# Performance work log

Measured on AMD Instinct MI355X. Metric: run time of the kernel, lower is better.

## Reference

```python
import jax, jax.numpy as jnp
import numpy as np
from functools import partial

D_MODEL = 1024
D_STATE = 16
D_CONV = 4
EXPAND = 2
D_INNER = EXPAND * D_MODEL
B = 2
L = 1024


def setup_inputs() -> dict:
    key = jax.random.key(0)
    ks = jax.random.split(key, 8)
    s = 0.02
    x = jax.random.normal(ks[0], (B, L, D_MODEL), dtype=jnp.float32)
    in_proj_w = jax.random.normal(ks[1], (D_MODEL, 2 * D_INNER), dtype=jnp.float32) * s
    conv_w = jax.random.normal(ks[2], (D_INNER, 1, D_CONV), dtype=jnp.float32) * s  # depthwise [out, in/groups, k]
    conv_b = jnp.zeros((D_INNER,), dtype=jnp.float32)
    x_proj_w = jax.random.normal(ks[3], (D_INNER, 2 * D_STATE), dtype=jnp.float32) * s
    dt_proj_w = jax.random.normal(ks[4], (D_INNER, D_INNER), dtype=jnp.float32) * s
    dt_proj_b = jax.random.normal(ks[5], (D_INNER,), dtype=jnp.float32) * s
    A_log = jnp.log(jnp.tile(jnp.arange(1, D_STATE + 1, dtype=jnp.float32), (D_INNER, 1)))  # [D_INNER, D_STATE]
    D_param = jnp.ones((D_INNER,), dtype=jnp.float32)
    out_proj_w = jax.random.normal(ks[6], (D_INNER, D_MODEL), dtype=jnp.float32) * s
    return {"x": x, "in_proj_w": in_proj_w, "conv_w": conv_w, "conv_b": conv_b,
            "x_proj_w": x_proj_w, "dt_proj_w": dt_proj_w, "dt_proj_b": dt_proj_b,
            "A_log": A_log, "D_param": D_param, "out_proj_w": out_proj_w}


def _selective_scan(u, delta, A, Bx, Cx, D_param):
    # u, delta: [B, L, D_INNER]; A: [D_INNER, N]; Bx, Cx: [B, L, N]
    deltaA = jnp.exp(delta[..., None] * A)                       # [B, L, D, N]
    deltaB_u = delta[..., None] * Bx[:, :, None, :] * u[..., None]  # [B, L, D, N]

    def step(h, inp):
        dA, dBu, c = inp  # dA,dBu: [B, D, N], c: [B, N]
        h = dA * h + dBu
        y = jnp.sum(h * c[:, None, :], axis=-1)  # [B, D]
        return h, y

    h0 = jnp.zeros((u.shape[0], u.shape[2], A.shape[1]), dtype=u.dtype)
    xs = (jnp.swapaxes(deltaA, 0, 1), jnp.swapaxes(deltaB_u, 0, 1), jnp.swapaxes(Cx, 0, 1))
    _, ys = jax.lax.scan(step, h0, xs)  # ys: [L, B, D]
    y = jnp.swapaxes(ys, 0, 1)
    return y + u * D_param


def reference(x, in_proj_w, conv_w, conv_b, x_proj_w, dt_proj_w, dt_proj_b, A_log, D_param, out_proj_w):
    xr = x @ in_proj_w                                   # [B, L, 2*D_INNER]
    u, res = xr[..., :D_INNER], xr[..., D_INNER:]
    # causal depthwise conv1d (padding=D_CONV-1 on the left, truncated to L)
    uc = jnp.swapaxes(u, 1, 2)                            # [B, D_INNER, L]
    uc = jax.lax.conv_general_dilated(
        uc, conv_w, window_strides=(1,), padding=[(D_CONV - 1, 0)],
        dimension_numbers=("NCH", "OIH", "NCH"), feature_group_count=D_INNER)
    uc = uc + conv_b[None, :, None]
    u = jax.nn.silu(jnp.swapaxes(uc, 1, 2))               # [B, L, D_INNER]
    x_dbl = u @ x_proj_w                                  # [B, L, 2*N]
    Bx, Cx = x_dbl[..., :D_STATE], x_dbl[..., D_STATE:]
    delta = jax.nn.softplus(u @ dt_proj_w.T + dt_proj_b)  # [B, L, D_INNER]
    A = -jnp.exp(A_log)
    y = _selective_scan(u, delta, A, Bx, Cx, D_param)
    y = y * jax.nn.silu(res)
    return y @ out_proj_w
```

## Files before the change

### kernel.cpp

```cpp
#include <hip/hip_runtime.h>
#include <math.h>

#define BATCH   2
#define LSEQ    1024
#define DMODEL  1024
#define DSTATE  16
#define DCONV   4
#define DINNER  2048
#define NROWS   (BATCH * LSEQ)

#define LCHUNK  32
#define NCHUNK  32

typedef short  bf16x8 __attribute__((ext_vector_type(8)));
typedef float  f32x4  __attribute__((ext_vector_type(4)));

__device__ __forceinline__ unsigned short f2bf(float f) {
  unsigned int u = __builtin_bit_cast(unsigned int, f);
  u = (u + 0x7fffu + ((u >> 16) & 1u)) >> 16;
  return (unsigned short)u;
}
__device__ __forceinline__ float bf2f(unsigned short h) {
  return __builtin_bit_cast(float, (unsigned int)h << 16);
}
__device__ __forceinline__ float softplus_f(float v) {
  return (v > 20.f) ? v : __logf(1.f + __expf(v));
}

__device__ __forceinline__ void cvt_ew_body(const float* __restrict__ s,
                                            unsigned short* __restrict__ d,
                                            int blk, int tid) {
  int i = blk * 256 + tid;
  float4 v = ((const float4*)s)[i];
  ushort4 o;
  o.x = f2bf(v.x); o.y = f2bf(v.y); o.z = f2bf(v.z); o.w = f2bf(v.w);
  ((ushort4*)d)[i] = o;
}

__device__ __forceinline__ void cvt_tr_body(const float* __restrict__ s,
                                            unsigned short* __restrict__ d,
                                            int R, int C, int c0, int r0,
                                            int tid, float (*T)[33]) {
#pragma unroll
  for (int i = 0; i < 4; ++i) {
    int e = tid + i * 256;
    int r = e >> 5, c = e & 31;
    T[r][c] = s[(size_t)(r0 + r) * C + c0 + c];
  }
  __syncthreads();
#pragma unroll
  for (int i = 0; i < 4; ++i) {
    int e = tid + i * 256;
    int c = e >> 5, r = e & 31;
    d[(size_t)(c0 + c) * R + r0 + r] = f2bf(T[r][c]);
  }
}

__global__ __launch_bounds__(256) void cvt_all(
    const float* __restrict__ x, const float* __restrict__ w_in,
    const float* __restrict__ dt_w, const float* __restrict__ out_w,
    unsigned short* __restrict__ XB, unsigned short* __restrict__ WINB,
    unsigned short* __restrict__ DTWB, unsigned short* __restrict__ OWB) {
  __shared__ float T[32][33];
  const int bid = blockIdx.x;
  const int tid = threadIdx.x;
  if (bid < 2048) {
    cvt_ew_body(x, XB, bid, tid);
  } else if (bid < 6144) {
    int t = bid - 2048;
    cvt_tr_body(w_in, WINB, 1024, 4096, (t & 127) * 32, (t >> 7) * 32, tid, T);
  } else if (bid < 10240) {
    cvt_ew_body(dt_w, DTWB, bid - 6144, tid);
  } else {
    int t = bid - 10240;
    cvt_tr_body(out_w, OWB, 2048, 1024, (t & 31) * 32, (t >> 5) * 32, tid, T);
  }
}

template <int BN>
__global__ __launch_bounds__(512) void mfma_gemm_nt(
    const unsigned short* __restrict__ A, int lda,
    const unsigned short* __restrict__ Bt, int ldb,
    void* __restrict__ C1v, int ld1,
    void* __restrict__ C2v, int ld2, int N1,
    const float* __restrict__ bias,
    int KS, int mode) {
  constexpr int NT = BN / 64;
  __shared__ unsigned short As[8 * 128 * 8];
  __shared__ unsigned short Bs[8 * BN * 8];
  const int tid  = threadIdx.x;
  const int wave = tid >> 6;
  const int lane = tid & 63;
  const int linear = blockIdx.y * gridDim.x + blockIdx.x;
  const int xcd = linear & 7;
  const int pos = linear >> 3;
  const int row0 = (xcd * 2 + (pos & 1)) * 128;
  const int col0 = (pos >> 1) * BN;
  const int wm0 = (wave >> 2) * 64;
  const int wn0 = (wave & 3) * (BN / 4);
  const int kb = blockIdx.z * KS;

  f32x4 acc[4][NT];
#pragma unroll
  for (int i = 0; i < 4; ++i)
#pragma unroll
    for (int j = 0; j < NT; ++j) acc[i][j] = (f32x4){0.f, 0.f, 0.f, 0.f};

  const int lkc = lane >> 4, li = lane & 15;
  const int sw = li & 7;
  for (int k0 = kb; k0 < kb + KS; k0 += 64) {
#pragma unroll
    for (int it = 0; it < 2; ++it) {
      int s = it * 512 + tid;
      int r = s >> 3;
      int kc = (s & 7) ^ (r & 7);
      __builtin_amdgcn_global_load_lds(
          (const __attribute__((address_space(1))) void*)(A + (size_t)(row0 + r) * lda + k0 + kc * 8),
          (__attribute__((address_space(3))) void*)(&As[s * 8]), 16, 0, 0);
    }
#pragma unroll
    for (int it = 0; it < BN / 64; ++it) {
      int s = it * 512 + tid;
      int r = s >> 3;
      int kc = (s & 7) ^ (r & 7);
      __builtin_amdgcn_global_load_lds(
          (const __attribute__((address_space(1))) void*)(Bt + (size_t)(col0 + r) * ldb + k0 + kc * 8),
          (__attribute__((address_space(3))) void*)(&Bs[s * 8]), 16, 0, 0);
    }
    __syncthreads();
#pragma unroll
    for (int half = 0; half < 2; ++half) {
      bf16x8 af[4], bfr[NT];
#pragma unroll
      for (int mt = 0; mt < 4; ++mt) {
        int ra = wm0 + mt * 16 + li;
        af[mt] = *(const bf16x8*)&As[(ra * 8 + ((half * 4 + lkc) ^ sw)) * 8];
      }
#pragma unroll
      for (int nt = 0; nt < NT; ++nt) {
        int rb = wn0 + nt * 16 + li;
        bfr[nt] = *(const bf16x8*)&Bs[(rb * 8 + ((half * 4 + lkc) ^ sw)) * 8];
      }
#pragma unroll
      for (int mt = 0; mt < 4; ++mt)
#pragma unroll
        for (int nt = 0; nt < NT; ++nt)
          acc[mt][nt] = __builtin_amdgcn_mfma_f32_16x16x32_bf16(
              af[mt], bfr[nt], acc[mt][nt], 0, 0, 0);
    }
    __syncthreads();
  }
  const int lq = lane >> 4;
#pragma unroll
  for (int mt = 0; mt < 4; ++mt) {
    int gm0 = row0 + wm0 + mt * 16 + lq * 4;
#pragma unroll
    for (int nt = 0; nt < NT; ++nt) {
      int gn = col0 + wn0 + nt * 16 + li;
      if (mode == 1) {
        if (gn < N1) {
          unsigned short* C1 = (unsigned short*)C1v;
#pragma unroll
          for (int r = 0; r < 4; ++r)
            C1[(size_t)(gm0 + r) * ld1 + gn] = f2bf(acc[mt][nt][r]);
        } else {
          unsigned short* C2 = (unsigned short*)C2v;
#pragma unroll
          for (int r = 0; r < 4; ++r)
            C2[(size_t)(gm0 + r) * ld2 + gn - N1] = f2bf(acc[mt][nt][r]);
        }
      } else {
        float* C1 = (float*)C1v + (size_t)blockIdx.z * (size_t)N1;
#pragma unroll
        for (int r = 0; r < 4; ++r)
          C1[(size_t)(gm0 + r) * ld1 + gn] = acc[mt][nt][r];
      }
    }
  }
}

__global__ __launch_bounds__(256) void out_reduce(
    const float* __restrict__ P, float* __restrict__ out) {
  const size_t SL = (size_t)NROWS * DMODEL;
  size_t i4 = (size_t)blockIdx.x * 256 + threadIdx.x;
  float4 a = ((const float4*)P)[i4];
  float4 b = ((const float4*)(P + SL))[i4];
  ((float4*)out)[i4] = make_float4(a.x + b.x, a.y + b.y, a.z + b.z, a.w + b.w);
}

__global__ __launch_bounds__(256) void conv_xproj(
    const unsigned short* __restrict__ UPREB, const float* __restrict__ cw,
    const float* __restrict__ cb, const float* __restrict__ W,
    unsigned short* __restrict__ UB, float* __restrict__ XPART) {
  const int ks = blockIdx.x;
  const int rt = blockIdx.y;
  const int row0 = rt * 16;
  const int kbase = ks * 256;
  __shared__ unsigned short sU[16][256];
  __shared__ float Bv[256 * 32];
  const int tid = threadIdx.x;

  for (int i = tid; i < 256 * 32; i += 256)
    Bv[i] = W[(size_t)(kbase + (i >> 5)) * 32 + (i & 31)];

  {
    const int d = kbase + tid;
    const float w0 = cw[d * DCONV + 0], w1 = cw[d * DCONV + 1];
    const float w2 = cw[d * DCONV + 2], w3 = cw[d * DCONV + 3];
    const float bias = cb[d];
    float x0, x1, x2;
    if ((row0 & (LSEQ - 1)) == 0) {
      x0 = x1 = x2 = 0.f;
    } else {
      x0 = bf2f(UPREB[(size_t)(row0 - 3) * DINNER + d]);
      x1 = bf2f(UPREB[(size_t)(row0 - 2) * DINNER + d]);
      x2 = bf2f(UPREB[(size_t)(row0 - 1) * DINNER + d]);
    }
    for (int r = 0; r < 16; ++r) {
      float x3 = bf2f(UPREB[(size_t)(row0 + r) * DINNER + d]);
      float a = bias + x0 * w0 + x1 * w1 + x2 * w2 + x3 * w3;
      float u = a / (1.f + __expf(-a));
      unsigned short ub = f2bf(u);
      sU[r][tid] = ub;
      UB[(size_t)(row0 + r) * DINNER + d] = ub;
      x0 = x1; x1 = x2; x2 = x3;
    }
  }
  __syncthreads();

  const int col = tid & 31, rg = tid >> 5;
  float acc[2] = {};
  for (int k = 0; k < 256; k += 2) {
    float b0 = Bv[k * 32 + col], b1 = Bv[(k + 1) * 32 + col];
#pragma unroll
    for (int rr = 0; rr < 2; ++rr) {
      ushort2 uv = *(const ushort2*)&sU[rg * 2 + rr][k];
      acc[rr] += bf2f(uv.x) * b0 + bf2f(uv.y) * b1;
    }
  }
#pragma unroll
  for (int rr = 0; rr < 2; ++rr)
    XPART[(size_t)ks * NROWS * 32 + (size_t)(row0 + rg * 2 + rr) * 32 + col] = acc[rr];
}

__global__ __launch_bounds__(256) void scan_pass1(
    const float* __restrict__ DT4, const float* __restrict__ dtb,
    const unsigned short* __restrict__ UB,
    const float* __restrict__ XPART, float* __restrict__ BCb,
    const float* __restrict__ A_log,
    float* __restrict__ PBUF, float* __restrict__ HBUF,
    unsigned short* __restrict__ DELTAB) {
  const int bx = blockIdx.x;
  const int b = bx >> 8;
  const int c = (bx >> 3) & (NCHUNK - 1);
  const int d = ((bx & 7) << 8) + threadIdx.x;
  const int l0 = c * LCHUNK;
  const size_t SL = (size_t)NROWS * DINNER;
  __shared__ float sB[LCHUNK * DSTATE];
#pragma unroll
  for (int i = 0; i < 2; ++i) {
    int e = threadIdx.x + i * 256;
    int row = e >> 4, col = e & 15;
    size_t base = (size_t)(b * LSEQ + l0 + row) * 32 + col;
    float s = 0.f;
#pragma unroll
    for (int ks = 0; ks < 8; ++ks) s += XPART[(size_t)ks * NROWS * 32 + base];
    sB[e] = s;
  }
  if ((bx & 7) == 0) {
#pragma unroll
    for (int i = 0; i < 4; ++i) {
      int e = threadIdx.x + i * 256;
      int row = e >> 5, col = e & 31;
      size_t base = (size_t)(b * LSEQ + l0 + row) * 32 + col;
      float s = 0.f;
#pragma unroll
      for (int ks = 0; ks < 8; ++ks) s += XPART[(size_t)ks * NROWS * 32 + base];
      BCb[base] = s;
    }
  }
  const float dtb_v = dtb[d];
  float Avv[DSTATE];
#pragma unroll
  for (int n = 0; n < DSTATE; ++n) Avv[n] = -__expf(A_log[d * DSTATE + n]);
  float h[DSTATE], P[DSTATE];
#pragma unroll
  for (int n = 0; n < DSTATE; ++n) { h[n] = 0.f; P[n] = 1.f; }
  __syncthreads();
  for (int lc = 0; lc < LCHUNK; ++lc) {
    size_t off = ((size_t)(b * LSEQ + l0 + lc)) * DINNER + d;
    float pre = DT4[off] + DT4[off + SL] + DT4[off + 2 * SL] + DT4[off + 3 * SL];
    unsigned short db = f2bf(softplus_f(pre + dtb_v));
    DELTAB[off] = db;
    float delta = bf2f(db);
    float du = delta * bf2f(UB[off]);
#pragma unroll
    for (int n = 0; n < DSTATE; ++n) {
      float dA = __expf(delta * Avv[n]);
      P[n] *= dA;
      h[n] = dA * h[n] + du * sB[lc * DSTATE + n];
    }
  }
  size_t base = ((size_t)(b * NCHUNK + c)) * DSTATE * DINNER + d;
#pragma unroll
  for (int n = 0; n < DSTATE; ++n) {
    PBUF[base + (size_t)n * DINNER] = P[n];
    HBUF[base + (size_t)n * DINNER] = h[n];
  }
}

__global__ __launch_bounds__(256) void scan_combine(
    const float* __restrict__ PBUF, float* __restrict__ HBUF) {
  const int bx = blockIdx.x;
  const int b = bx >> 7;
  const int n = (bx >> 3) & (DSTATE - 1);
  const int d = ((bx & 7) << 8) + threadIdx.x;
  float h = 0.f;
  for (int c = 0; c < NCHUNK; ++c) {
    size_t idx = (((size_t)(b * NCHUNK + c)) * DSTATE + n) * DINNER + d;
    float p = PBUF[idx];
    float hl = HBUF[idx];
    HBUF[idx] = h;
    h = p * h + hl;
  }
}

__global__ __launch_bounds__(256) void scan_pass2(
    const unsigned short* __restrict__ DELTAB, const unsigned short* __restrict__ UB,
    const float* __restrict__ BC, const float* __restrict__ HBUF,
    const float* __restrict__ A_log, const float* __restrict__ D_param,
    const unsigned short* __restrict__ RESB, unsigned short* __restrict__ YB) {
  const int bx = blockIdx.x;
  const int b = bx >> 8;
  const int c = (bx >> 3) & (NCHUNK - 1);
  const int d = ((bx & 7) << 8) + threadIdx.x;
  const int l0 = c * LCHUNK;
  __shared__ float sBC[LCHUNK * 32];
#pragma unroll
  for (int i = 0; i < 4; ++i) {
    int e = threadIdx.x + i * 256;
    sBC[e] = BC[((size_t)(b * LSEQ + l0 + (e >> 5))) * 32 + (e & 31)];
  }
  float Avv[DSTATE];
#pragma unroll
  for (int n = 0; n < DSTATE; ++n) Avv[n] = -__expf(A_log[d * DSTATE + n]);
  const float Dp = D_param[d];
  float h[DSTATE];
  size_t base = ((size_t)(b * NCHUNK + c)) * DSTATE * DINNER + d;
#pragma unroll
  for (int n = 0; n < DSTATE; ++n) h[n] = HBUF[base + (size_t)n * DINNER];
  __syncthreads();
  for (int lc = 0; lc < LCHUNK; ++lc) {
    size_t off = ((size_t)(b * LSEQ + l0 + lc)) * DINNER + d;
    float delta = bf2f(DELTAB[off]);
    float uu = bf2f(UB[off]);
    float du = delta * uu;
    float y = 0.f;
#pragma unroll
    for (int n = 0; n < DSTATE; ++n) {
      float dA = __expf(delta * Avv[n]);
      h[n] = dA * h[n] + du * sBC[lc * 32 + n];
      y += h[n] * sBC[lc * 32 + 16 + n];
    }
    y += uu * Dp;
    float r = bf2f(RESB[off]);
    YB[off] = f2bf(y * (r / (1.f + __expf(-r))));
  }
}

extern "C" void kernel_launch(void* const* d_in, const int* in_sizes, int n_in,
                              void* d_out, int out_size, void* d_ws, size_t ws_size,
                              hipStream_t stream) {
  const float* x       = (const float*)d_in[0];
  const float* w_in    = (const float*)d_in[1];
  const float* conv_w  = (const float*)d_in[2];
  const float* conv_b  = (const float*)d_in[3];
  const float* xproj_w = (const float*)d_in[4];
  const float* dt_w    = (const float*)d_in[5];
  const float* dt_b    = (const float*)d_in[6];
  const float* A_log   = (const float*)d_in[7];
  const float* D_par   = (const float*)d_in[8];
  const float* out_w   = (const float*)d_in[9];
  float* out = (float*)d_out;

  char* ws = (char*)d_ws;
  const size_t MB = 1024 * 1024;
  unsigned short* UPREB  = (unsigned short*)(ws + 0 * MB);
  unsigned short* RESB   = (unsigned short*)(ws + 8 * MB);
  unsigned short* UB     = (unsigned short*)(ws + 16 * MB);
  unsigned short* DELTAB = (unsigned short*)(ws + 24 * MB);
  unsigned short* YB     = (unsigned short*)(ws + 32 * MB);
  unsigned short* XB     = (unsigned short*)(ws + 40 * MB);
  unsigned short* WINB   = (unsigned short*)(ws + 44 * MB);
  unsigned short* DTWB   = (unsigned short*)(ws + 52 * MB);
  unsigned short* OWB    = (unsigned short*)(ws + 60 * MB);
  float* PBUF  = (float*)(ws + 0 * MB);
  float* HBUF  = (float*)(ws + 40 * MB);
  float* BCb   = (float*)(ws + 48 * MB);
  float* XPART = (float*)(ws + 48 * MB + 512 * 1024);
  float* OUT2  = (float*)(ws + 128 * MB);
  float* DT4   = (float*)(ws + 64 * MB);

  cvt_all<<<dim3(12288), dim3(256), 0, stream>>>(
      x, w_in, dt_w, out_w, XB, WINB, DTWB, OWB);
  mfma_gemm_nt<128><<<dim3(2 * DINNER / 128, NROWS / 128, 1), dim3(512), 0, stream>>>(
      XB, DMODEL, WINB, DMODEL, UPREB, DINNER, RESB, DINNER, DINNER,
      nullptr, DMODEL, 1);
  conv_xproj<<<dim3(8, NROWS / 16), dim3(256), 0, stream>>>(
      UPREB, conv_w, conv_b, xproj_w, UB, XPART);
  mfma_gemm_nt<128><<<dim3(DINNER / 128, NROWS / 128, 4), dim3(512), 0, stream>>>(
      UB, DINNER, DTWB, DINNER, DT4, DINNER, nullptr, 0, NROWS * DINNER,
      nullptr, DINNER / 4, 3);
  scan_pass1<<<dim3(BATCH * NCHUNK * (DINNER / 256)), dim3(256), 0, stream>>>(
      DT4, dt_b, UB, XPART, BCb, A_log, PBUF, HBUF, DELTAB);
  scan_combine<<<dim3(BATCH * DSTATE * (DINNER / 256)), dim3(256), 0, stream>>>(PBUF, HBUF);
  scan_pass2<<<dim3(BATCH * NCHUNK * (DINNER / 256)), dim3(256), 0, stream>>>(
      DELTAB, UB, BCb, HBUF, A_log, D_par, RESB, YB);
  mfma_gemm_nt<64><<<dim3(DMODEL / 64, NROWS / 128, 2), dim3(512), 0, stream>>>(
      YB, DINNER, OWB, DINNER, OUT2, DMODEL, nullptr, 0, NROWS * DMODEL,
      nullptr, DINNER / 2, 3);
  out_reduce<<<dim3(2048), dim3(256), 0, stream>>>(OUT2, out);
}
```

Measured before the change: 263.0 us.

## Replace split-K dt_proj GEMM with dedicated 64x64 GEMM fusing bias+softplus epilogue

The dt_proj GEMM previously used a 4-way split-K that wrote four fp32 partial slabs, which scan_pass1 then summed before applying bias, softplus and bf16 rounding. A new 64x64-tile MFMA kernel now covers the full K in one pass and applies bias, softplus and bf16 conversion in its epilogue, writing DELTAB directly. scan_pass1 just reads DELTAB. This removes about 64MB of fp32 partial traffic and the reduction, at the cost of a smaller tile and a longer K loop per block with a single LDS buffer and no double buffering.

```diff
diff --git a/kernel.cpp b/kernel.cpp
--- a/kernel.cpp
+++ b/kernel.cpp
@@ -179,6 +179,78 @@
   }
 }
 
+__global__ __launch_bounds__(512) void mfma_gemm_dt(
+    const unsigned short* __restrict__ A, int lda,
+    const unsigned short* __restrict__ Bt, int ldb,
+    unsigned short* __restrict__ C, int ldc,
+    const float* __restrict__ bias, int KS) {
+  __shared__ unsigned short As[8 * 64 * 8];
+  __shared__ unsigned short Bs[8 * 64 * 8];
+  const int tid  = threadIdx.x;
+  const int wave = tid >> 6;
+  const int lane = tid & 63;
+  const int total = gridDim.x * gridDim.y;
+  const int lin = blockIdx.y * gridDim.x + blockIdx.x;
+  const int wg = (lin & 7) * (total >> 3) + (lin >> 3);
+  const int row0 = (wg / gridDim.x) * 64;
+  const int col0 = (wg % gridDim.x) * 64;
+  const int wm0 = (wave >> 2) * 32;
+  const int wn0 = (wave & 3) * 16;
+
+  f32x4 acc[2];
+  acc[0] = (f32x4){0.f, 0.f, 0.f, 0.f};
+  acc[1] = (f32x4){0.f, 0.f, 0.f, 0.f};
+
+  const int lkc = lane >> 4, li = lane & 15;
+  const int sw = li & 7;
+  for (int k0 = 0; k0 < KS; k0 += 64) {
+    {
+      int s = tid;
+      int r = s >> 3;
+      int kc = (s & 7) ^ (r & 7);
+      __builtin_amdgcn_global_load_lds(
+          (const __attribute__((address_space(1))) void*)(A + (size_t)(row0 + r) * lda + k0 + kc * 8),
+          (__attribute__((address_space(3))) void*)(&As[s * 8]), 16, 0, 0);
+    }
+    {
+      int s = tid;
+      int r = s >> 3;
+      int kc = (s & 7) ^ (r & 7);
+      __builtin_amdgcn_global_load_lds(
+          (const __attribute__((address_space(1))) void*)(Bt + (size_t)(col0 + r) * ldb + k0 + kc * 8),
+          (__attribute__((address_space(3))) void*)(&Bs[s * 8]), 16, 0, 0);
+    }
+    __syncthreads();
+#pragma unroll
+    for (int half = 0; half < 2; ++half) {
+      bf16x8 af[2], bfr;
+#pragma unroll
+      for (int mt = 0; mt < 2; ++mt) {
+        int ra = wm0 + mt * 16 + li;
+        af[mt] = *(const bf16x8*)&As[(ra * 8 + ((half * 4 + lkc) ^ sw)) * 8];
+      }
+      {
+        int rb = wn0 + li;
+        bfr = *(const bf16x8*)&Bs[(rb * 8 + ((half * 4 + lkc) ^ sw)) * 8];
+      }
+#pragma unroll
+      for (int mt = 0; mt < 2; ++mt)
+        acc[mt] = __builtin_amdgcn_mfma_f32_16x16x32_bf16(af[mt], bfr, acc[mt], 0, 0, 0);
+    }
+    __syncthreads();
+  }
+  const int lq = lane >> 4;
+  const int gn = col0 + wn0 + li;
+  const float bb = bias[gn];
+#pragma unroll
+  for (int mt = 0; mt < 2; ++mt) {
+    int gm0 = row0 + wm0 + mt * 16 + lq * 4;
+#pragma unroll
+    for (int r = 0; r < 4; ++r)
+      C[(size_t)(gm0 + r) * ldc + gn] = f2bf(softplus_f(acc[mt][r] + bb));
+  }
+}
+
 __global__ __launch_bounds__(256) void out_reduce(
     const float* __restrict__ P, float* __restrict__ out) {
   const size_t SL = (size_t)NROWS * DMODEL;
@@ -244,18 +316,15 @@
 }
 
 __global__ __launch_bounds__(256) void scan_pass1(
-    const float* __restrict__ DT4, const float* __restrict__ dtb,
-    const unsigned short* __restrict__ UB,
+    const unsigned short* __restrict__ DELTAB, const unsigned short* __restrict__ UB,
     const float* __restrict__ XPART, float* __restrict__ BCb,
     const float* __restrict__ A_log,
-    float* __restrict__ PBUF, float* __restrict__ HBUF,
-    unsigned short* __restrict__ DELTAB) {
+    float* __restrict__ PBUF, float* __restrict__ HBUF) {
   const int bx = blockIdx.x;
   const int b = bx >> 8;
   const int c = (bx >> 3) & (NCHUNK - 1);
   const int d = ((bx & 7) << 8) + threadIdx.x;
   const int l0 = c * LCHUNK;
-  const size_t SL = (size_t)NROWS * DINNER;
   __shared__ float sB[LCHUNK * DSTATE];
 #pragma unroll
   for (int i = 0; i < 2; ++i) {
@@ -279,7 +348,6 @@
       BCb[base] = s;
     }
   }
-  const float dtb_v = dtb[d];
   float Avv[DSTATE];
 #pragma unroll
   for (int n = 0; n < DSTATE; ++n) Avv[n] = -__expf(A_log[d * DSTATE + n]);
@@ -289,10 +357,7 @@
   __syncthreads();
   for (int lc = 0; lc < LCHUNK; ++lc) {
     size_t off = ((size_t)(b * LSEQ + l0 + lc)) * DINNER + d;
-    float pre = DT4[off] + DT4[off + SL] + DT4[off + 2 * SL] + DT4[off + 3 * SL];
-    unsigned short db = f2bf(softplus_f(pre + dtb_v));
-    DELTAB[off] = db;
-    float delta = bf2f(db);
+    float delta = bf2f(DELTAB[off]);
     float du = delta * bf2f(UB[off]);
 #pragma unroll
     for (int n = 0; n < DSTATE; ++n) {
@@ -398,8 +463,7 @@
   float* HBUF  = (float*)(ws + 40 * MB);
   float* BCb   = (float*)(ws + 48 * MB);
   float* XPART = (float*)(ws + 48 * MB + 512 * 1024);
-  float* OUT2  = (float*)(ws + 128 * MB);
-  float* DT4   = (float*)(ws + 64 * MB);
+  float* OUT2  = (float*)(ws + 40 * MB);
 
   cvt_all<<<dim3(12288), dim3(256), 0, stream>>>(
       x, w_in, dt_w, out_w, XB, WINB, DTWB, OWB);
@@ -408,11 +472,10 @@
       nullptr, DMODEL, 1);
   conv_xproj<<<dim3(8, NROWS / 16), dim3(256), 0, stream>>>(
       UPREB, conv_w, conv_b, xproj_w, UB, XPART);
-  mfma_gemm_nt<128><<<dim3(DINNER / 128, NROWS / 128, 4), dim3(512), 0, stream>>>(
-      UB, DINNER, DTWB, DINNER, DT4, DINNER, nullptr, 0, NROWS * DINNER,
-      nullptr, DINNER / 4, 3);
+  mfma_gemm_dt<<<dim3(DINNER / 64, NROWS / 64, 1), dim3(512), 0, stream>>>(
+      UB, DINNER, DTWB, DINNER, DELTAB, DINNER, dt_b, DINNER);
   scan_pass1<<<dim3(BATCH * NCHUNK * (DINNER / 256)), dim3(256), 0, stream>>>(
-      DT4, dt_b, UB, XPART, BCb, A_log, PBUF, HBUF, DELTAB);
+      DELTAB, UB, XPART, BCb, A_log, PBUF, HBUF);
   scan_combine<<<dim3(BATCH * DSTATE * (DINNER / 256)), dim3(256), 0, stream>>>(PBUF, HBUF);
   scan_pass2<<<dim3(BATCH * NCHUNK * (DINNER / 256)), dim3(256), 0, stream>>>(
       DELTAB, UB, BCb, HBUF, A_log, D_par, RESB, YB);
```

Result: faster. 249.0 us (-5.3%).
